# Kernel tuning notes

Measured on AMD Instinct MI355X. Metric: run time of the kernel, lower is better.

Reference implementation:

```python
import jax, jax.numpy as jnp
import numpy as np

B, N1, N2, C, COUT, NS = 2, 8192, 8192, 128, 128, 16


def leaky(x):
    return jnp.where(x >= 0, x, 0.1 * x)


def group_norm(x, gamma, beta, groups, eps=1e-5):
    # x: [B, C, N]
    b, c, n = x.shape
    xg = x.reshape(b, groups, (c // groups) * n)
    mu = xg.mean(-1, keepdims=True)
    var = xg.var(-1, keepdims=True)
    xg = (xg - mu) * jax.lax.rsqrt(var + eps)
    return xg.reshape(b, c, n) * gamma[None, :, None] + beta[None, :, None]


def knn_point(nsample, xyz_t, new_xyz_t):
    # xyz_t: [B,N2,3] source, new_xyz_t: [B,N1,3] queries -> idx [B,N1,nsample]
    s_new = jnp.sum(new_xyz_t * new_xyz_t, -1)  # [B,N1]
    s_src = jnp.sum(xyz_t * xyz_t, -1)          # [B,N2]
    d = s_new[:, :, None] + s_src[:, None, :] - 2.0 * jnp.einsum('bnc,bmc->bnm', new_xyz_t, xyz_t)
    _, idx = jax.lax.top_k(-d, nsample)
    return idx


def index_points(points, idx):
    # points: [B,N,C], idx: [B,N1,S] -> [B,N1,S,C]
    return jax.vmap(lambda p, i: p[i])(points, idx)


def setup_inputs() -> dict:
    key = jax.random.key(0)
    ks = jax.random.split(key, 16)
    rn = lambda k, s, sc=1.0: jax.random.normal(k, s, jnp.float32) * sc
    return {
        'xyz1': rn(ks[0], (B, 3, N1)),
        'xyz2': rn(ks[1], (B, 3, N2)),
        'feat1': rn(ks[2], (B, C, N1)),
        'feat2': rn(ks[3], (B, C, N2)),
        'pos_w': rn(ks[4], (C, 3), 0.2), 'pos_b': jnp.zeros(C), 'pos_g': jnp.ones(C), 'pos_beta': jnp.zeros(C),
        'ek_w': rn(ks[5], (C, 3), 0.2), 'ek_b': jnp.zeros(C),
        'eq_w': rn(ks[6], (C, 3), 0.2), 'eq_b': jnp.zeros(C),
        'ev1_w': rn(ks[7], (C, 3), 0.2), 'ev1_b': jnp.zeros(C),
        'ev2_w': rn(ks[8], (C, 3), 0.2), 'ev2_b': jnp.zeros(C),
        'qk_w': rn(ks[9], (C, C), 0.05),
        'v_w': rn(ks[10], (C, C), 0.05),
        'ff_w': rn(ks[11], (COUT, C), 0.05), 'ff_b': jnp.zeros(COUT), 'ff_g': jnp.ones(COUT), 'ff_beta': jnp.zeros(COUT),
        'nsample': NS,
    }


def reference(xyz1, xyz2, feat1, feat2, pos_w, pos_b, pos_g, pos_beta,
              ek_w, ek_b, eq_w, eq_b, ev1_w, ev1_b, ev2_w, ev2_b,
              qk_w, v_w, ff_w, ff_b, ff_g, ff_beta, nsample):
    c = pos_w.shape[0]
    # positional encoder: conv1d 3->C, GN(C//16), LeakyReLU(0.1)
    def pos_enc(xyz):
        h = jnp.einsum('dc,bcn->bdn', pos_w, xyz) + pos_b[None, :, None]
        return leaky(group_norm(h, pos_g, pos_beta, c // 16))
    feat1 = feat1 + pos_enc(xyz1)
    feat2 = feat2 + pos_enc(xyz2)

    xyz1_t = xyz1.transpose(0, 2, 1)
    xyz2_t = xyz2.transpose(0, 2, 1)
    idx = knn_point(nsample, xyz2_t, xyz1_t)  # [B,N1,S]

    xyz2_s = index_points(xyz2_t, idx).transpose(0, 3, 1, 2)   # [B,3,N1,S]
    real_xyz = xyz2_s - xyz1[:, :, :, None]                     # [B,3,N1,S]

    def enc(w, b):
        return leaky(jnp.einsum('dc,bcns->bdns', w, real_xyz) + b[None, :, None, None])
    ekc, eqc, ev1c, ev2c = enc(ek_w, ek_b), enc(eq_w, eq_b), enc(ev1_w, ev1_b), enc(ev2_w, ev2_b)

    feat2_s = index_points(feat2.transpose(0, 2, 1), idx).transpose(0, 3, 1, 2)  # [B,C,N1,S]

    q = jnp.einsum('dc,bcns->bdns', qk_w, feat1[:, :, :, None] * eqc)
    k = feat2_s * ekc
    v = jnp.einsum('dc,bcns->bdns', v_w, feat2_s * ev1c) * ev2c

    atten = jnp.einsum('bcns,bcns->bns', q, k) / float(np.sqrt(c))
    atten = jax.nn.softmax(atten, axis=-1)
    feat_new = jnp.einsum('bcns,bns->bcn', v, atten)
    feat_new = feat_new + feat1  # skip connection

    h = jnp.einsum('dc,bcn->bdn', ff_w, feat_new) + ff_b[None, :, None]
    feat_new = leaky(group_norm(h, ff_g, ff_beta, ff_w.shape[0] // 16))
    return (xyz1, feat_new)
```

## Files before the change

kernel.cpp:

```cpp
#include <hip/hip_runtime.h>
#include <hip/hip_bf16.h>

#define BB  2
#define NN1 8192
#define NN2 8192
#define CC  128
#define SS  16

typedef unsigned short u16;
typedef unsigned int u32;
typedef short bf16x8 __attribute__((ext_vector_type(8)));
typedef float f32x4  __attribute__((ext_vector_type(4)));

__device__ __forceinline__ u16 f2bf(float f) {
  __hip_bfloat16 h = __float2bfloat16(f);
  return *(u16*)&h;
}
__device__ __forceinline__ float bf2f(u16 u) {
  union { float f; unsigned int u; } v; v.u = ((unsigned int)u) << 16;
  return v.f;
}
__device__ __forceinline__ float bflo(u32 w) {
  union { float f; unsigned int u; } v; v.u = w << 16; return v.f;
}
__device__ __forceinline__ float bfhi(u32 w) {
  union { float f; unsigned int u; } v; v.u = w & 0xFFFF0000u; return v.f;
}
__device__ __forceinline__ float leaky(float x) { return x >= 0.0f ? x : 0.1f * x; }

__global__ __launch_bounds__(256)
void k_prep(const float* __restrict__ qkw, const float* __restrict__ vw,
            u16* __restrict__ oa, u16* __restrict__ ob,
            const float* __restrict__ xyz1, const float* __restrict__ xyz2,
            float4* __restrict__ px1, float4* __restrict__ px2,
            float* __restrict__ mom_part) {
  int bx = blockIdx.x, t = threadIdx.x;
  if (bx < 128) {
    int e = bx * 256 + t;
    if (e < 16384) oa[e] = f2bf(qkw[e]);
    else ob[e - 16384] = f2bf(vw[e - 16384]);
    return;
  }
  __shared__ float wred[4][9];
  const float* xyz; float4* px; int e;
  if (bx < 192) { e = (bx - 128) * 256 + t; xyz = xyz1; px = px1; }
  else          { e = (bx - 192) * 256 + t; xyz = xyz2; px = px2; }
  int b = e >> 13, n = e & 8191;
  float x = xyz[(b * 3 + 0) * 8192 + n];
  float y = xyz[(b * 3 + 1) * 8192 + n];
  float z = xyz[(b * 3 + 2) * 8192 + n];
  px[e] = make_float4(x, y, z, x * x + y * y + z * z);
  float s[9] = { x, y, z, x * x, y * y, z * z, x * y, x * z, y * z };
#pragma unroll
  for (int o = 1; o < 64; o <<= 1)
#pragma unroll
    for (int i = 0; i < 9; ++i) s[i] += __shfl_xor(s[i], o);
  int w = t >> 6;
  if ((t & 63) == 0)
#pragma unroll
    for (int i = 0; i < 9; ++i) wred[w][i] = s[i];
  __syncthreads();
  if (t < 9) {
    float tot = wred[0][t] + wred[1][t] + wred[2][t] + wred[3][t];
    mom_part[(bx - 128) * 9 + t] = tot;
  }
}

__global__ __launch_bounds__(512)
void k_gnstats(const float* __restrict__ mom_part, const float* __restrict__ pw,
               const float* __restrict__ pb, float2* __restrict__ gnp) {
  int t = threadIdx.x;
  int cl = t >> 8, b = (t >> 7) & 1, c = t & 127;
  const float* P = mom_part + (cl * 64 + b * 32) * 9;
  float M[9];
#pragma unroll
  for (int i = 0; i < 9; ++i) {
    float sum = 0.0f;
    for (int k = 0; k < 32; ++k) sum += P[k * 9 + i];
    M[i] = sum;
  }
  const float inv = 1.0f / 8192.0f;
  float mx = M[0] * inv, my = M[1] * inv, mz = M[2] * inv;
  float sxx = M[3] * inv, syy = M[4] * inv, szz = M[5] * inv;
  float sxy = M[6] * inv, sxz = M[7] * inv, syz = M[8] * inv;
  float w0 = pw[c * 3], w1 = pw[c * 3 + 1], w2 = pw[c * 3 + 2], bc = pb[c];
  float wm = w0 * mx + w1 * my + w2 * mz;
  float Eh = wm + bc;
  float wSw = w0 * w0 * sxx + w1 * w1 * syy + w2 * w2 * szz
            + 2.0f * (w0 * w1 * sxy + w0 * w2 * sxz + w1 * w2 * syz);
  float Eh2 = wSw + 2.0f * bc * wm + bc * bc;
#pragma unroll
  for (int o = 1; o < 16; o <<= 1) { Eh += __shfl_xor(Eh, o); Eh2 += __shfl_xor(Eh2, o); }
  if ((c & 15) == 0) {
    float mu = Eh * 0.0625f;
    float var = Eh2 * 0.0625f - mu * mu;
    gnp[cl * 16 + b * 8 + (c >> 4)] = make_float2(mu, rsqrtf(var + 1e-5f));
  }
}


__device__ __forceinline__ u32 knnkey(float4 qv, float4 c, u32 idx) {
  float m = fmaf(qv.x, c.x, fmaf(qv.y, c.y, qv.z * c.z));
  float d = fmaf(-2.0f, m, qv.w + c.w);
  d = fmaxf(d, 0.0f);
  return (__float_as_uint(d) & 0xFFFFE000u) | idx;
}

__device__ __forceinline__ void ce_x(u32& v, int j, bool up, int l) {
  u32 p = __shfl_xor(v, j);
  u32 mn = v < p ? v : p;
  u32 mx = v < p ? p : v;
  bool lower = ((l & j) == 0);
  v = (lower == up) ? mn : mx;
}

__device__ __forceinline__ void sort128(u32& v0, u32& v1, int l) {
#pragma unroll
  for (int k = 2; k <= 64; k <<= 1) {
#pragma unroll
    for (int j = k >> 1; j > 0; j >>= 1) {
      ce_x(v0, j, ((l & k) == 0), l);
      ce_x(v1, j, (((l + 64) & k) == 0), l);
    }
  }
  { u32 mn = v0 < v1 ? v0 : v1; u32 mx = v0 < v1 ? v1 : v0; v0 = mn; v1 = mx; }
#pragma unroll
  for (int j = 32; j > 0; j >>= 1) {
    ce_x(v0, j, true, l);
    ce_x(v1, j, true, l);
  }
}

__global__ __launch_bounds__(256)
void k_pk(const float4* __restrict__ px1, const float4* __restrict__ px2,
          int* __restrict__ idxout,
          const float* __restrict__ xyz1, const float* __restrict__ xyz2,
          const float* __restrict__ feat1, const float* __restrict__ feat2,
          const float* __restrict__ pw, const float* __restrict__ pb,
          const float* __restrict__ gam, const float* __restrict__ bet,
          const float2* __restrict__ gnp,
          float* __restrict__ outf, u16* __restrict__ outb) {
  __shared__ float smem[128 * 17];
  int bx = blockIdx.x, t = threadIdx.x;

  if (bx < 4096) {
    int w = t >> 6, l = t & 63;
    int q = bx * 4 + w;
    int b = q >> 13;
    float4 qv = px1[q];
    const float4* cp = px2 + (b << 13);
    u32* wb = ((u32*)smem) + w * 128;
    u32 kth = 0xFFFFFFFFu;
    int cnt = 0;
    const unsigned long long below = (1ull << l) - 1ull;
    float4 c_cur = cp[l];
    for (int it = 0; it < 128; ++it) {
      float4 c_nxt = c_cur;
      if (it < 127) c_nxt = cp[(it + 1) * 64 + l];
      u32 key = knnkey(qv, c_cur, (u32)(it * 64 + l));
      bool pass = key < kth;
      unsigned long long mask = __ballot(pass);
      if (mask) {
        int off = cnt + (int)__popcll(mask & below);
        if (pass) wb[off] = key;
        cnt += (int)__popcll(mask);
        if (cnt > 64) {
          u32 v0 = (l < cnt) ? wb[l] : 0xFFFFFFFFu;
          u32 v1 = (64 + l < cnt) ? wb[64 + l] : 0xFFFFFFFFu;
          sort128(v0, v1, l);
          if (l < 16) wb[l] = v0;
          cnt = 16;
          kth = __shfl(v0, 15);
        }
      }
      c_cur = c_nxt;
    }
    u32 v0 = (l < cnt) ? wb[l] : 0xFFFFFFFFu;
    u32 v1 = (64 + l < cnt) ? wb[64 + l] : 0xFFFFFFFFu;
    sort128(v0, v1, l);
    if (l < 16) idxout[q * 16 + l] = (int)(v0 & 8191u);
    return;
  }

  bx -= 4096;
  const float* xyz; const float* feat; const float2* gp; int asbf;
  if (bx < 1024) { xyz = xyz1; feat = feat1; gp = gnp;      asbf = 0; }
  else           { xyz = xyz2; feat = feat2; gp = gnp + 16; asbf = 1; bx -= 1024; }
  const int N = 8192;
  int b = bx / 512, n0 = (bx % 512) * 16;
  for (int it = 0; it < 8; ++it) {
    int j = t & 15, c = it * 16 + (t >> 4);
    smem[c * 17 + j] = feat[(b * 128 + c) * N + n0 + j];
  }
  int c = t & 127;
  float w0 = pw[c * 3], w1 = pw[c * 3 + 1], w2 = pw[c * 3 + 2], bc = pb[c];
  float2 g2 = gp[b * 8 + (c >> 4)];
  float gm = gam[c], b2 = bet[c];
  __syncthreads();
  for (int it = 0; it < 8; ++it) {
    int j = it * 2 + (t >> 7);
    int n = n0 + j;
    float xs = xyz[(b * 3 + 0) * N + n];
    float ys = xyz[(b * 3 + 1) * N + n];
    float zs = xyz[(b * 3 + 2) * N + n];
    float hv = w0 * xs + w1 * ys + w2 * zs + bc;
    float xo = (hv - g2.x) * g2.y * gm + b2;
    float r = smem[c * 17 + j] + leaky(xo);
    if (asbf) outb[(size_t)(b * N + n) * 128 + c] = f2bf(r);
    else      outf[(size_t)(b * N + n) * 128 + c] = r;
  }
}

__device__ __forceinline__ float4 ld_enc(const float* encS, int e, int c) {
  int xe = e ^ ((c >> 3) & 3);
  return *(const float4*)&encS[c * 16 + xe * 4];
}

__global__ __launch_bounds__(256, 2)
void k_attn(const float4* __restrict__ px1, const float4* __restrict__ px2,
            const float* __restrict__ f1p, const u16* __restrict__ f2p,
            const int* __restrict__ idxb,
            const u16* __restrict__ wq, const u16* __restrict__ wvm,
            const float* __restrict__ eqw, const float* __restrict__ eqb,
            const float* __restrict__ ekw, const float* __restrict__ ekb,
            const float* __restrict__ ev1w, const float* __restrict__ ev1b,
            const float* __restrict__ ev2w, const float* __restrict__ ev2b,
            float* __restrict__ outp) {
  const int t = threadIdx.x, bx = blockIdx.x;
  const int b = bx >> 10;
  const int base8 = (bx & 1023) * 8;
  const int w = t >> 6, l = t & 63, l15 = l & 15, l4 = l >> 4;

  __shared__ float encS[128 * 16];
  __shared__ float f1s[8 * 132];
  __shared__ float4 e3S[128];
  __shared__ float4 relS[8 * 16];

  for (int i = t; i < 384; i += 256) {
    int e = i >> 7, c = i & 127;
    const float* wsrc = (e == 0) ? eqw : (e == 1) ? ekw : ev1w;
    const float* bsrc = (e == 0) ? eqb : (e == 1) ? ekb : ev1b;
    int xe = e ^ ((c >> 3) & 3);
    float* dst = &encS[c * 16 + xe * 4];
    dst[0] = wsrc[c * 3]; dst[1] = wsrc[c * 3 + 1];
    dst[2] = wsrc[c * 3 + 2]; dst[3] = bsrc[c];
  }
  if (t < 128)
    e3S[t] = make_float4(ev2w[t * 3], ev2w[t * 3 + 1], ev2w[t * 3 + 2], ev2b[t]);
  for (int i = t; i < 1024; i += 256) {
    int p = i >> 7, c = i & 127;
    f1s[p * 132 + c] = f1p[(size_t)(b * NN1 + base8 + p) * 128 + c];
  }

  const int pt0 = base8 + w * 2, pt1 = pt0 + 1;
  const int j0 = idxb[(b * NN1 + pt0) * 16 + l15];
  const int j1 = idxb[(b * NN1 + pt1) * 16 + l15];
  float4 qc0 = px1[b * NN1 + pt0];
  float4 qc1 = px1[b * NN1 + pt1];
  float4 cc0 = px2[b * NN2 + j0];
  float4 cc1 = px2[b * NN2 + j1];
  float r0[2], r1[2], r2[2];
  r0[0] = cc0.x - qc0.x; r1[0] = cc0.y - qc0.y; r2[0] = cc0.z - qc0.z;
  r0[1] = cc1.x - qc1.x; r1[1] = cc1.y - qc1.y; r2[1] = cc1.z - qc1.z;

  const u16* row0 = f2p + (size_t)(b * NN2 + j0) * 128;
  const u16* row1 = f2p + (size_t)(b * NN2 + j1) * 128;
  __syncthreads();

  bf16x8 bq[2][4];
#pragma unroll
  for (int ks = 0; ks < 4; ++ks) {
#pragma unroll
    for (int j = 0; j < 8; ++j) {
      int c = ks * 32 + l4 * 8 + j;
      float4 ew = ld_enc(encS, 0, c);
      float f10 = f1s[(w * 2 + 0) * 132 + c];
      float f11 = f1s[(w * 2 + 1) * 132 + c];
      float e0 = leaky(ew.x * r0[0] + ew.y * r1[0] + ew.z * r2[0] + ew.w);
      float e1 = leaky(ew.x * r0[1] + ew.y * r1[1] + ew.z * r2[1] + ew.w);
      bq[0][ks][j] = (short)f2bf(f10 * e0);
      bq[1][ks][j] = (short)f2bf(f11 * e1);
    }
  }

  float dp0 = 0.0f, dp1 = 0.0f;
  uint2 kc0 = *(const uint2*)(row0 + l4 * 4);
  uint2 kc1 = *(const uint2*)(row1 + l4 * 4);
#pragma unroll
  for (int mt = 0; mt < 8; ++mt) {
    uint2 kn0 = kc0, kn1 = kc1;
    if (mt < 7) {
      kn0 = *(const uint2*)(row0 + (mt + 1) * 16 + l4 * 4);
      kn1 = *(const uint2*)(row1 + (mt + 1) * 16 + l4 * 4);
    }
    f32x4 a0 = (f32x4){0.f, 0.f, 0.f, 0.f};
    f32x4 a1 = (f32x4){0.f, 0.f, 0.f, 0.f};
#pragma unroll
    for (int ks = 0; ks < 4; ++ks) {
      bf16x8 af = *(const bf16x8*)&wq[(mt * 16 + l15) * 128 + ks * 32 + l4 * 8];
      a0 = __builtin_amdgcn_mfma_f32_16x16x32_bf16(af, bq[0][ks], a0, 0, 0, 0);
      a1 = __builtin_amdgcn_mfma_f32_16x16x32_bf16(af, bq[1][ks], a1, 0, 0, 0);
    }
    float f2v0[4] = { bflo(kc0.x), bfhi(kc0.x), bflo(kc0.y), bfhi(kc0.y) };
    float f2v1[4] = { bflo(kc1.x), bfhi(kc1.x), bflo(kc1.y), bfhi(kc1.y) };
#pragma unroll
    for (int r = 0; r < 4; ++r) {
      int c = mt * 16 + l4 * 4 + r;
      float4 ew = ld_enc(encS, 1, c);
      float ek0 = leaky(ew.x * r0[0] + ew.y * r1[0] + ew.z * r2[0] + ew.w);
      float ek1 = leaky(ew.x * r0[1] + ew.y * r1[1] + ew.z * r2[1] + ew.w);
      dp0 += a0[r] * (f2v0[r] * ek0);
      dp1 += a1[r] * (f2v1[r] * ek1);
    }
    kc0 = kn0; kc1 = kn1;
  }

  bf16x8 fB[2][4];
#pragma unroll
  for (int ks = 0; ks < 4; ++ks) {
    fB[0][ks] = *(const bf16x8*)(row0 + ks * 32 + l4 * 8);
    fB[1][ks] = *(const bf16x8*)(row1 + ks * 32 + l4 * 8);
  }

  dp0 += __shfl_xor(dp0, 16); dp0 += __shfl_xor(dp0, 32);
  dp1 += __shfl_xor(dp1, 16); dp1 += __shfl_xor(dp1, 32);
  float aw0, aw1;
  {
    float x = dp0 * 0.08838834764831845f;
    float m = x;
#pragma unroll
    for (int o = 1; o < 16; o <<= 1) m = fmaxf(m, __shfl_xor(m, o));
    float e = __expf(x - m);
    float s = e;
#pragma unroll
    for (int o = 1; o < 16; o <<= 1) s += __shfl_xor(s, o);
    aw0 = e / s;
  }
  {
    float x = dp1 * 0.08838834764831845f;
    float m = x;
#pragma unroll
    for (int o = 1; o < 16; o <<= 1) m = fmaxf(m, __shfl_xor(m, o));
    float e = __expf(x - m);
    float s = e;
#pragma unroll
    for (int o = 1; o < 16; o <<= 1) s += __shfl_xor(s, o);
    aw1 = e / s;
  }

  if (l < 16) {
    relS[(w * 2 + 0) * 16 + l] = make_float4(r0[0], r1[0], r2[0], aw0);
    relS[(w * 2 + 1) * 16 + l] = make_float4(r0[1], r1[1], r2[1], aw1);
  }

  bf16x8 bv[2][4];
#pragma unroll
  for (int ks = 0; ks < 4; ++ks) {
#pragma unroll
    for (int j = 0; j < 8; ++j) {
      int c = ks * 32 + l4 * 8 + j;
      float4 ew = ld_enc(encS, 2, c);
      float e0 = leaky(ew.x * r0[0] + ew.y * r1[0] + ew.z * r2[0] + ew.w);
      float e1 = leaky(ew.x * r0[1] + ew.y * r1[1] + ew.z * r2[1] + ew.w);
      bv[0][ks][j] = (short)f2bf(bf2f((u16)fB[0][ks][j]) * e0);
      bv[1][ks][j] = (short)f2bf(bf2f((u16)fB[1][ks][j]) * e1);
    }
  }

#pragma unroll
  for (int mt = 0; mt < 8; ++mt) {
    f32x4 a0 = (f32x4){0.f, 0.f, 0.f, 0.f};
    f32x4 a1 = (f32x4){0.f, 0.f, 0.f, 0.f};
#pragma unroll
    for (int ks = 0; ks < 4; ++ks) {
      bf16x8 bf = *(const bf16x8*)&wvm[(mt * 16 + l15) * 128 + ks * 32 + l4 * 8];
      a0 = __builtin_amdgcn_mfma_f32_16x16x32_bf16(bv[0][ks], bf, a0, 0, 0, 0);
      a1 = __builtin_amdgcn_mfma_f32_16x16x32_bf16(bv[1][ks], bf, a1, 0, 0, 0);
    }
    const int m = mt * 16 + l15;
    float4 ew = e3S[m];
    float acc0 = 0.0f, acc1 = 0.0f;
#pragma unroll
    for (int r = 0; r < 4; ++r) {
      float4 ra = relS[(w * 2 + 0) * 16 + l4 * 4 + r];
      float4 rb = relS[(w * 2 + 1) * 16 + l4 * 4 + r];
      float e0 = leaky(ew.x * ra.x + ew.y * ra.y + ew.z * ra.z + ew.w);
      float e1 = leaky(ew.x * rb.x + ew.y * rb.y + ew.z * rb.z + ew.w);
      acc0 += a0[r] * e0 * ra.w;
      acc1 += a1[r] * e1 * rb.w;
    }
    acc0 += __shfl_xor(acc0, 16); acc0 += __shfl_xor(acc0, 32);
    acc1 += __shfl_xor(acc1, 16); acc1 += __shfl_xor(acc1, 32);
    if (l < 16) {
      outp[(size_t)(b * NN1 + pt0) * 128 + m] = acc0 + f1s[(w * 2 + 0) * 132 + m];
      outp[(size_t)(b * NN1 + pt1) * 128 + m] = acc1 + f1s[(w * 2 + 1) * 132 + m];
    }
  }
}

__global__ __launch_bounds__(256)
void k_ff(const float* __restrict__ xin, const float* __restrict__ ffw,
          const float* __restrict__ ffb, float* __restrict__ hout,
          float* __restrict__ pstat) {
  int t = threadIdx.x, bx = blockIdx.x;
  int b = bx / (NN1 / 32), n0 = (bx % (NN1 / 32)) * 32;
  __shared__ float XT[128][34];
  for (int e = t; e < 4096; e += 256) {
    int c = e & 127, nn = e >> 7;
    XT[c][nn] = xin[(b * NN1 + n0 + nn) * 128 + c];
  }
  __syncthreads();
  int d = t >> 1, nh = t & 1;
  float acc[16];
#pragma unroll
  for (int j = 0; j < 16; ++j) acc[j] = 0.0f;
  for (int c0 = 0; c0 < 128; c0 += 4) {
    float4 w4 = *(const float4*)&ffw[d * 128 + c0];
    const float wa[4] = { w4.x, w4.y, w4.z, w4.w };
#pragma unroll
    for (int k = 0; k < 4; ++k) {
      int c = c0 + k;
#pragma unroll
      for (int j2 = 0; j2 < 8; ++j2) {
        float2 xv = *(const float2*)&XT[c][nh * 16 + j2 * 2];
        acc[j2 * 2 + 0] += wa[k] * xv.x;
        acc[j2 * 2 + 1] += wa[k] * xv.y;
      }
    }
  }
  float bias = ffb[d];
  float ls = 0.0f, lss = 0.0f;
  float out[16];
#pragma unroll
  for (int j = 0; j < 16; ++j) { float h = acc[j] + bias; out[j] = h; ls += h; lss += h * h; }
#pragma unroll
  for (int j4 = 0; j4 < 4; ++j4) {
    float4 o = { out[j4 * 4], out[j4 * 4 + 1], out[j4 * 4 + 2], out[j4 * 4 + 3] };
    *(float4*)&hout[(b * 128 + d) * NN1 + n0 + nh * 16 + j4 * 4] = o;
  }
#pragma unroll
  for (int o = 1; o <= 16; o <<= 1) { ls += __shfl_xor(ls, o); lss += __shfl_xor(lss, o); }
  if ((t & 31) == 0) {
    int g = t >> 5;
    pstat[bx * 16 + g * 2 + 0] = ls;
    pstat[bx * 16 + g * 2 + 1] = lss;
  }
}

__global__ __launch_bounds__(512)
void k_ffred(const float* __restrict__ pstat, float* __restrict__ gnf) {
  __shared__ float red[512];
  int t = threadIdx.x;
  int b = t >> 8, i = t & 15, chunk = (t >> 4) & 15;
  float s = 0.0f;
#pragma unroll
  for (int k = 0; k < 16; ++k)
    s += pstat[(b * 256 + chunk * 16 + k) * 16 + i];
  red[t] = s;
  __syncthreads();
  if (chunk == 0) {
    float tot = 0.0f;
#pragma unroll
    for (int k2 = 0; k2 < 16; ++k2) tot += red[(b << 8) | (k2 << 4) | i];
    gnf[b * 16 + i] = tot;
  }
}

__global__ __launch_bounds__(256)
void k_final(const float* __restrict__ h, const float* __restrict__ gnf,
             const float* __restrict__ g, const float* __restrict__ bt,
             const float* __restrict__ xyz1, float* __restrict__ out) {
  int bx = blockIdx.x;
  if (bx >= 8192) {
    int e = (bx - 8192) * 256 + threadIdx.x;
    out[e] = xyz1[e];
    return;
  }
  int e = bx * 256 + threadIdx.x;
  int d = (e / NN1) & 127;
  int b = e / (128 * NN1);
  int gi = b * 16 + (d >> 4) * 2;
  float cnt = 16.0f * (float)NN1;
  float mu = gnf[gi] / cnt;
  float var = gnf[gi + 1] / cnt - mu * mu;
  float rs = rsqrtf(var + 1e-5f);
  float x = (h[e] - mu) * rs * g[d] + bt[d];
  out[BB * 3 * NN1 + e] = leaky(x);
}

extern "C" void kernel_launch(void* const* d_in, const int* in_sizes, int n_in,
                              void* d_out, int out_size, void* d_ws, size_t ws_size,
                              hipStream_t stream) {
  const float* xyz1   = (const float*)d_in[0];
  const float* xyz2   = (const float*)d_in[1];
  const float* feat1  = (const float*)d_in[2];
  const float* feat2  = (const float*)d_in[3];
  const float* pos_w  = (const float*)d_in[4];
  const float* pos_b  = (const float*)d_in[5];
  const float* pos_g  = (const float*)d_in[6];
  const float* pos_bt = (const float*)d_in[7];
  const float* ek_w   = (const float*)d_in[8];
  const float* ek_b   = (const float*)d_in[9];
  const float* eq_w   = (const float*)d_in[10];
  const float* eq_b   = (const float*)d_in[11];
  const float* ev1_w  = (const float*)d_in[12];
  const float* ev1_b  = (const float*)d_in[13];
  const float* ev2_w  = (const float*)d_in[14];
  const float* ev2_b  = (const float*)d_in[15];
  const float* qk_w   = (const float*)d_in[16];
  const float* v_w    = (const float*)d_in[17];
  const float* ff_w   = (const float*)d_in[18];
  const float* ff_b   = (const float*)d_in[19];
  const float* ff_g   = (const float*)d_in[20];
  const float* ff_bt  = (const float*)d_in[21];
  (void)in_sizes; (void)n_in; (void)out_size; (void)ws_size;

  char* ws = (char*)d_ws;
  float*  feat1p   = (float*)(ws);
  u16*    feat2pb  = (u16*)  (ws + 8388608);
  float*  attn_out = (float*)(ws + 12582912);
  float*  h_ff     = (float*)(ws + 20971520);
  int*    idxb     = (int*)  (ws + 29360128);
  u16*    wqk      = (u16*)  (ws + 30408704);
  u16*    wv       = (u16*)  (ws + 30441472);
  float*  mom_part = (float*)(ws + 30474240);
  float2* gnp      = (float2*)(ws + 30478848);
  float*  pstat    = (float*)(ws + 30479104);
  float*  gnf      = (float*)(ws + 30511872);
  float4* px1      = (float4*)(ws + 30512000);
  float4* px2      = (float4*)(ws + 30774144);

  k_prep<<<256, 256, 0, stream>>>(qk_w, v_w, wqk, wv, xyz1, xyz2, px1, px2, mom_part);
  k_gnstats<<<1, 512, 0, stream>>>(mom_part, pos_w, pos_b, gnp);
  k_pk<<<6144, 256, 0, stream>>>(px1, px2, idxb, xyz1, xyz2, feat1, feat2,
                                 pos_w, pos_b, pos_g, pos_bt, gnp, feat1p, feat2pb);
  k_attn<<<2048, 256, 0, stream>>>(px1, px2, feat1p, feat2pb, idxb, wqk, wv,
                                   eq_w, eq_b, ek_w, ek_b, ev1_w, ev1_b, ev2_w, ev2_b,
                                   attn_out);
  k_ff<<<512, 256, 0, stream>>>(attn_out, ff_w, ff_b, h_ff, pstat);
  k_ffred<<<1, 512, 0, stream>>>(pstat, gnf);
  k_final<<<8384, 256, 0, stream>>>(h_ff, gnf, ff_g, ff_bt, xyz1, (float*)d_out);
}
```

Baseline: 216.5 us.

## Run feed-forward conv on bf16 MFMA and store attention output as bf16

The feed-forward 128x128 projection is rewritten from a scalar FP32 shared-memory GEMM into a bf16 MFMA kernel with 64 points per block. The weights are converted to bf16 in the prep kernel, and the attention kernel now writes its output in bf16 to halve that intermediate's traffic. The attention kernel also drops the manual k-prefetch and builds the v-operand fragments right after the k loop, and the partial-stats reduction is adjusted for the new block count. This trades some precision in the FF input and weights for less memory traffic and matrix-core throughput. The hout stores are now strided per point.

Result: faster. 208.4 us (-3.8%).

```diff
diff --git a/kernel.cpp b/kernel.cpp
--- a/kernel.cpp
+++ b/kernel.cpp
@@ -30,21 +30,23 @@
 
 __global__ __launch_bounds__(256)
 void k_prep(const float* __restrict__ qkw, const float* __restrict__ vw,
-            u16* __restrict__ oa, u16* __restrict__ ob,
+            const float* __restrict__ ffw,
+            u16* __restrict__ oa, u16* __restrict__ ob, u16* __restrict__ of,
             const float* __restrict__ xyz1, const float* __restrict__ xyz2,
             float4* __restrict__ px1, float4* __restrict__ px2,
             float* __restrict__ mom_part) {
   int bx = blockIdx.x, t = threadIdx.x;
-  if (bx < 128) {
+  if (bx < 192) {
     int e = bx * 256 + t;
     if (e < 16384) oa[e] = f2bf(qkw[e]);
-    else ob[e - 16384] = f2bf(vw[e - 16384]);
+    else if (e < 32768) ob[e - 16384] = f2bf(vw[e - 16384]);
+    else of[e - 32768] = f2bf(ffw[e - 32768]);
     return;
   }
   __shared__ float wred[4][9];
   const float* xyz; float4* px; int e;
-  if (bx < 192) { e = (bx - 128) * 256 + t; xyz = xyz1; px = px1; }
-  else          { e = (bx - 192) * 256 + t; xyz = xyz2; px = px2; }
+  if (bx < 256) { e = (bx - 192) * 256 + t; xyz = xyz1; px = px1; }
+  else          { e = (bx - 256) * 256 + t; xyz = xyz2; px = px2; }
   int b = e >> 13, n = e & 8191;
   float x = xyz[(b * 3 + 0) * 8192 + n];
   float y = xyz[(b * 3 + 1) * 8192 + n];
@@ -62,7 +64,7 @@
   __syncthreads();
   if (t < 9) {
     float tot = wred[0][t] + wred[1][t] + wred[2][t] + wred[3][t];
-    mom_part[(bx - 128) * 9 + t] = tot;
+    mom_part[(bx - 192) * 9 + t] = tot;
   }
 }
 
@@ -225,7 +227,7 @@
             const float* __restrict__ ekw, const float* __restrict__ ekb,
             const float* __restrict__ ev1w, const float* __restrict__ ev1b,
             const float* __restrict__ ev2w, const float* __restrict__ ev2b,
-            float* __restrict__ outp) {
+            u16* __restrict__ outp) {
   const int t = threadIdx.x, bx = blockIdx.x;
   const int b = bx >> 10;
   const int base8 = (bx & 1023) * 8;
@@ -284,15 +286,10 @@
   }
 
   float dp0 = 0.0f, dp1 = 0.0f;
-  uint2 kc0 = *(const uint2*)(row0 + l4 * 4);
-  uint2 kc1 = *(const uint2*)(row1 + l4 * 4);
 #pragma unroll
   for (int mt = 0; mt < 8; ++mt) {
-    uint2 kn0 = kc0, kn1 = kc1;
-    if (mt < 7) {
-      kn0 = *(const uint2*)(row0 + (mt + 1) * 16 + l4 * 4);
-      kn1 = *(const uint2*)(row1 + (mt + 1) * 16 + l4 * 4);
-    }
+    uint2 kc0 = *(const uint2*)(row0 + mt * 16 + l4 * 4);
+    uint2 kc1 = *(const uint2*)(row1 + mt * 16 + l4 * 4);
     f32x4 a0 = (f32x4){0.f, 0.f, 0.f, 0.f};
     f32x4 a1 = (f32x4){0.f, 0.f, 0.f, 0.f};
 #pragma unroll
@@ -312,14 +309,22 @@
       dp0 += a0[r] * (f2v0[r] * ek0);
       dp1 += a1[r] * (f2v1[r] * ek1);
     }
-    kc0 = kn0; kc1 = kn1;
-  }
-
-  bf16x8 fB[2][4];
+  }
+
+  bf16x8 bv[2][4];
 #pragma unroll
   for (int ks = 0; ks < 4; ++ks) {
-    fB[0][ks] = *(const bf16x8*)(row0 + ks * 32 + l4 * 8);
-    fB[1][ks] = *(const bf16x8*)(row1 + ks * 32 + l4 * 8);
+    bf16x8 fb0 = *(const bf16x8*)(row0 + ks * 32 + l4 * 8);
+    bf16x8 fb1 = *(const bf16x8*)(row1 + ks * 32 + l4 * 8);
+#pragma unroll
+    for (int j = 0; j < 8; ++j) {
+      int c = ks * 32 + l4 * 8 + j;
+      float4 ew = ld_enc(encS, 2, c);
+      float e0 = leaky(ew.x * r0[0] + ew.y * r1[0] + ew.z * r2[0] + ew.w);
+      float e1 = leaky(ew.x * r0[1] + ew.y * r1[1] + ew.z * r2[1] + ew.w);
+      bv[0][ks][j] = (short)f2bf(bf2f((u16)fb0[j]) * e0);
+      bv[1][ks][j] = (short)f2bf(bf2f((u16)fb1[j]) * e1);
+    }
   }
 
   dp0 += __shfl_xor(dp0, 16); dp0 += __shfl_xor(dp0, 32);
@@ -351,20 +356,6 @@
   if (l < 16) {
     relS[(w * 2 + 0) * 16 + l] = make_float4(r0[0], r1[0], r2[0], aw0);
     relS[(w * 2 + 1) * 16 + l] = make_float4(r0[1], r1[1], r2[1], aw1);
-  }
-
-  bf16x8 bv[2][4];
-#pragma unroll
-  for (int ks = 0; ks < 4; ++ks) {
-#pragma unroll
-    for (int j = 0; j < 8; ++j) {
-      int c = ks * 32 + l4 * 8 + j;
-      float4 ew = ld_enc(encS, 2, c);
-      float e0 = leaky(ew.x * r0[0] + ew.y * r1[0] + ew.z * r2[0] + ew.w);
-      float e1 = leaky(ew.x * r0[1] + ew.y * r1[1] + ew.z * r2[1] + ew.w);
-      bv[0][ks][j] = (short)f2bf(bf2f((u16)fB[0][ks][j]) * e0);
-      bv[1][ks][j] = (short)f2bf(bf2f((u16)fB[1][ks][j]) * e1);
-    }
   }
 
 #pragma unroll
@@ -392,58 +383,69 @@
     acc0 += __shfl_xor(acc0, 16); acc0 += __shfl_xor(acc0, 32);
     acc1 += __shfl_xor(acc1, 16); acc1 += __shfl_xor(acc1, 32);
     if (l < 16) {
-      outp[(size_t)(b * NN1 + pt0) * 128 + m] = acc0 + f1s[(w * 2 + 0) * 132 + m];
-      outp[(size_t)(b * NN1 + pt1) * 128 + m] = acc1 + f1s[(w * 2 + 1) * 132 + m];
+      outp[(size_t)(b * NN1 + pt0) * 128 + m] =
+          f2bf(acc0 + f1s[(w * 2 + 0) * 132 + m]);
+      outp[(size_t)(b * NN1 + pt1) * 128 + m] =
+          f2bf(acc1 + f1s[(w * 2 + 1) * 132 + m]);
     }
   }
 }
 
 __global__ __launch_bounds__(256)
-void k_ff(const float* __restrict__ xin, const float* __restrict__ ffw,
+void k_ff(const u16* __restrict__ xb, const u16* __restrict__ wfb,
           const float* __restrict__ ffb, float* __restrict__ hout,
           float* __restrict__ pstat) {
-  int t = threadIdx.x, bx = blockIdx.x;
-  int b = bx / (NN1 / 32), n0 = (bx % (NN1 / 32)) * 32;
-  __shared__ float XT[128][34];
-  for (int e = t; e < 4096; e += 256) {
-    int c = e & 127, nn = e >> 7;
-    XT[c][nn] = xin[(b * NN1 + n0 + nn) * 128 + c];
-  }
+  const int t = threadIdx.x, bx = blockIdx.x;
+  const int w = t >> 6, l = t & 63, l15 = l & 15, l4 = l >> 4;
+  __shared__ float bS[128];
+  __shared__ float red[4][16];
+  if (t < 128) bS[t] = ffb[t];
+  const int pt = bx * 64 + w * 16 + l15;
+  const int b = pt >> 13, n = pt & 8191;
+  const u16* row = xb + (size_t)pt * 128;
+  bf16x8 bfrag[4];
+#pragma unroll
+  for (int ks = 0; ks < 4; ++ks)
+    bfrag[ks] = *(const bf16x8*)(row + ks * 32 + l4 * 8);
   __syncthreads();
-  int d = t >> 1, nh = t & 1;
-  float acc[16];
-#pragma unroll
-  for (int j = 0; j < 16; ++j) acc[j] = 0.0f;
-  for (int c0 = 0; c0 < 128; c0 += 4) {
-    float4 w4 = *(const float4*)&ffw[d * 128 + c0];
-    const float wa[4] = { w4.x, w4.y, w4.z, w4.w };
-#pragma unroll
-    for (int k = 0; k < 4; ++k) {
-      int c = c0 + k;
-#pragma unroll
-      for (int j2 = 0; j2 < 8; ++j2) {
-        float2 xv = *(const float2*)&XT[c][nh * 16 + j2 * 2];
-        acc[j2 * 2 + 0] += wa[k] * xv.x;
-        acc[j2 * 2 + 1] += wa[k] * xv.y;
-      }
-    }
-  }
-  float bias = ffb[d];
-  float ls = 0.0f, lss = 0.0f;
-  float out[16];
-#pragma unroll
-  for (int j = 0; j < 16; ++j) { float h = acc[j] + bias; out[j] = h; ls += h; lss += h * h; }
-#pragma unroll
-  for (int j4 = 0; j4 < 4; ++j4) {
-    float4 o = { out[j4 * 4], out[j4 * 4 + 1], out[j4 * 4 + 2], out[j4 * 4 + 3] };
-    *(float4*)&hout[(b * 128 + d) * NN1 + n0 + nh * 16 + j4 * 4] = o;
-  }
-#pragma unroll
-  for (int o = 1; o <= 16; o <<= 1) { ls += __shfl_xor(ls, o); lss += __shfl_xor(lss, o); }
-  if ((t & 31) == 0) {
-    int g = t >> 5;
-    pstat[bx * 16 + g * 2 + 0] = ls;
-    pstat[bx * 16 + g * 2 + 1] = lss;
+  float gs[8], gss[8];
+#pragma unroll
+  for (int mt = 0; mt < 8; ++mt) {
+    f32x4 a = (f32x4){0.f, 0.f, 0.f, 0.f};
+#pragma unroll
+    for (int ks = 0; ks < 4; ++ks) {
+      bf16x8 af = *(const bf16x8*)&wfb[(mt * 16 + l15) * 128 + ks * 32 + l4 * 8];
+      a = __builtin_amdgcn_mfma_f32_16x16x32_bf16(af, bfrag[ks], a, 0, 0, 0);
+    }
+    int d0 = mt * 16 + l4 * 4;
+    float s = 0.0f, ss = 0.0f;
+#pragma unroll
+    for (int r = 0; r < 4; ++r) {
+      float h = a[r] + bS[d0 + r];
+      hout[(size_t)(b * 128 + d0 + r) * 8192 + n] = h;
+      s += h; ss += h * h;
+    }
+    gs[mt] = s; gss[mt] = ss;
+  }
+#pragma unroll
+  for (int mt = 0; mt < 8; ++mt) {
+#pragma unroll
+    for (int o = 1; o < 64; o <<= 1) {
+      gs[mt] += __shfl_xor(gs[mt], o);
+      gss[mt] += __shfl_xor(gss[mt], o);
+    }
+  }
+  if (l == 0) {
+#pragma unroll
+    for (int mt = 0; mt < 8; ++mt) {
+      red[w][mt * 2 + 0] = gs[mt];
+      red[w][mt * 2 + 1] = gss[mt];
+    }
+  }
+  __syncthreads();
+  if (t < 16) {
+    float tot = red[0][t] + red[1][t] + red[2][t] + red[3][t];
+    pstat[bx * 16 + t] = tot;
   }
 }
 
@@ -454,8 +456,8 @@
   int b = t >> 8, i = t & 15, chunk = (t >> 4) & 15;
   float s = 0.0f;
 #pragma unroll
-  for (int k = 0; k < 16; ++k)
-    s += pstat[(b * 256 + chunk * 16 + k) * 16 + i];
+  for (int k = 0; k < 8; ++k)
+    s += pstat[(b * 128 + chunk * 8 + k) * 16 + i];
   red[t] = s;
   __syncthreads();
   if (chunk == 0) {
@@ -518,26 +520,28 @@
   char* ws = (char*)d_ws;
   float*  feat1p   = (float*)(ws);
   u16*    feat2pb  = (u16*)  (ws + 8388608);
-  float*  attn_out = (float*)(ws + 12582912);
-  float*  h_ff     = (float*)(ws + 20971520);
-  int*    idxb     = (int*)  (ws + 29360128);
-  u16*    wqk      = (u16*)  (ws + 30408704);
-  u16*    wv       = (u16*)  (ws + 30441472);
-  float*  mom_part = (float*)(ws + 30474240);
-  float2* gnp      = (float2*)(ws + 30478848);
-  float*  pstat    = (float*)(ws + 30479104);
-  float*  gnf      = (float*)(ws + 30511872);
-  float4* px1      = (float4*)(ws + 30512000);
-  float4* px2      = (float4*)(ws + 30774144);
-
-  k_prep<<<256, 256, 0, stream>>>(qk_w, v_w, wqk, wv, xyz1, xyz2, px1, px2, mom_part);
+  u16*    attn_out = (u16*)  (ws + 12582912);
+  float*  h_ff     = (float*)(ws + 16777216);
+  int*    idxb     = (int*)  (ws + 25165824);
+  u16*    wqk      = (u16*)  (ws + 26214400);
+  u16*    wv       = (u16*)  (ws + 26247168);
+  u16*    wff      = (u16*)  (ws + 26279936);
+  float*  mom_part = (float*)(ws + 26312704);
+  float2* gnp      = (float2*)(ws + 26317312);
+  float*  pstat    = (float*)(ws + 26317568);
+  float*  gnf      = (float*)(ws + 26333952);
+  float4* px1      = (float4*)(ws + 26334080);
+  float4* px2      = (float4*)(ws + 26596224);
+
+  k_prep<<<320, 256, 0, stream>>>(qk_w, v_w, ff_w, wqk, wv, wff,
+                                  xyz1, xyz2, px1, px2, mom_part);
   k_gnstats<<<1, 512, 0, stream>>>(mom_part, pos_w, pos_b, gnp);
   k_pk<<<6144, 256, 0, stream>>>(px1, px2, idxb, xyz1, xyz2, feat1, feat2,
                                  pos_w, pos_b, pos_g, pos_bt, gnp, feat1p, feat2pb);
   k_attn<<<2048, 256, 0, stream>>>(px1, px2, feat1p, feat2pb, idxb, wqk, wv,
                                    eq_w, eq_b, ek_w, ek_b, ev1_w, ev1_b, ev2_w, ev2_b,
                                    attn_out);
-  k_ff<<<512, 256, 0, stream>>>(attn_out, ff_w, ff_b, h_ff, pstat);
+  k_ff<<<256, 256, 0, stream>>>(attn_out, wff, ff_b, h_ff, pstat);
   k_ffred<<<1, 512, 0, stream>>>(pstat, gnf);
   k_final<<<8384, 256, 0, stream>>>(h_ff, gnf, ff_g, ff_bt, xyz1, (float*)d_out);
 }
```
